# Kernel optimization log

Measured on AMD Instinct MI355X. Metric: run time of the kernel, lower is better.

Reference implementation:

```python
import jax, jax.numpy as jnp
import numpy as np

NUM_NODES = 20000
NUM_RELATIONS = 32
HIDDEN = 128
EMB = 16
NUM_EDGES = 600000


def setup_inputs() -> dict:
    key = jax.random.key(0)
    ks = jax.random.split(key, 8)
    edge_index = jax.random.randint(ks[0], (2, NUM_EDGES), 0, NUM_NODES, dtype=jnp.int64)
    edge_type = jax.random.randint(ks[1], (NUM_EDGES,), 0, NUM_RELATIONS, dtype=jnp.int64)
    node_emb = jax.random.normal(ks[2], (NUM_NODES, EMB), dtype=jnp.float32)
    W1 = jax.random.normal(ks[3], (NUM_RELATIONS, EMB, HIDDEN), dtype=jnp.float32) * (1.0 / np.sqrt(EMB))
    root1 = jax.random.normal(ks[4], (EMB, HIDDEN), dtype=jnp.float32) * (1.0 / np.sqrt(EMB))
    b1 = jnp.zeros((HIDDEN,), dtype=jnp.float32)
    W2 = jax.random.normal(ks[5], (NUM_RELATIONS, HIDDEN, HIDDEN), dtype=jnp.float32) * (1.0 / np.sqrt(HIDDEN))
    root2 = jax.random.normal(ks[6], (HIDDEN, HIDDEN), dtype=jnp.float32) * (1.0 / np.sqrt(HIDDEN))
    b2 = jnp.zeros((HIDDEN,), dtype=jnp.float32)
    return {"edge_index": edge_index, "edge_type": edge_type, "node_emb": node_emb,
            "W1": W1, "root1": root1, "b1": b1, "W2": W2, "root2": root2, "b2": b2}


def rgcn_layer(x, edge_index, edge_type, W, root, bias):
    # PyG RGCNConv: per-relation transform, per-(dst, relation) MEAN aggregation,
    # summed over relations, plus root transform and bias.
    src, dst = edge_index[0], edge_index[1]
    # mean normalization per (dst, relation) segment
    seg = dst * NUM_RELATIONS + edge_type                      # [E]
    counts = jax.ops.segment_sum(jnp.ones(seg.shape, jnp.float32), seg,
                                 num_segments=NUM_NODES * NUM_RELATIONS)
    inv = jnp.where(counts > 0, 1.0 / counts, 0.0)
    # transform every node by every relation weight: [N, R, H]
    xr = jnp.einsum('nf,rfh->nrh', x, W)
    msg = xr[src, edge_type] * inv[seg][:, None]               # [E, H]
    agg = jax.ops.segment_sum(msg, dst, num_segments=NUM_NODES)  # [N, H]
    return agg + x @ root + bias


def reference(edge_index, edge_type, node_emb, W1, root1, b1, W2, root2, b2):
    h = rgcn_layer(node_emb, edge_index, edge_type, W1, root1, b1)
    h = jax.nn.relu(h)
    h = rgcn_layer(h, edge_index, edge_type, W2, root2, b2)
    return h
```

## Files before the change

### kernel.cpp

```cpp
#include <hip/hip_runtime.h>
#include <hip/hip_bf16.h>

#define N_NODES 20000
#define N_REL 32
#define HID 128
#define EMB 16
#define N_EDGES 600000
#define NB (N_NODES * N_REL)

typedef __attribute__((ext_vector_type(8))) short  bf8v;
typedef __attribute__((ext_vector_type(8))) unsigned short us8v;
typedef __attribute__((ext_vector_type(4))) float  f4v;

__device__ __forceinline__ unsigned short f2b(float f) {
    __hip_bfloat16 h = __float2bfloat16(f);
    return __builtin_bit_cast(unsigned short, h);
}
__device__ __forceinline__ float b2f(unsigned short u) {
    unsigned int x = ((unsigned int)u) << 16;
    return __builtin_bit_cast(float, x);
}

__device__ __forceinline__ void lds_barrier() {
    asm volatile("s_waitcnt lgkmcnt(0)\n\ts_barrier" ::: "memory");
}

#define R_W2 (N_REL * HID * HID)
#define R_XB (N_NODES * EMB)
#define R_W1 (N_REL * EMB * HID)
#define R_R1 (HID * 32)
#define R_R2 (HID * HID)
#define R_HIST N_EDGES
#define PRE_TOT (R_W2 + R_XB + R_W1 + R_R1 + R_R2 + R_HIST)

__global__ __launch_bounds__(256) void pre1_k(
    const int* __restrict__ dst, const int* __restrict__ et,
    const float* __restrict__ x, const float* __restrict__ W1,
    const float* __restrict__ root1, const float* __restrict__ W2,
    const float* __restrict__ root2,
    int* __restrict__ hist,
    unsigned short* __restrict__ xb, unsigned short* __restrict__ w1t,
    unsigned short* __restrict__ r1t, unsigned short* __restrict__ w2t,
    unsigned short* __restrict__ r2t) {
    int i = blockIdx.x * 256 + threadIdx.x;
    if (i < R_W2) {
        int r = i >> 14, k = (i >> 7) & 127, n = i & 127;
        int kb = r * 4 + (k >> 5), q = (k >> 3) & 3, j = k & 7;
        int ct8 = n >> 4, m16 = n & 15;
        w2t[(size_t)kb * 4096 + ct8 * 512 + m16 * 32 + q * 8 + j] = f2b(W2[i]);
        return;
    }
    i -= R_W2;
    if (i < R_XB) { xb[i] = f2b(x[i]); return; }
    i -= R_XB;
    if (i < R_W1) {
        int rel = i >> 11, kk = (i >> 7) & 15, n = i & 127;
        int kb = rel >> 1, k = ((rel & 1) << 4) + kk;
        int q = k >> 3, j = k & 7, ct8 = n >> 4, m16 = n & 15;
        w1t[kb * 4096 + ct8 * 512 + m16 * 32 + q * 8 + j] = f2b(W1[i]);
        return;
    }
    i -= R_W1;
    if (i < R_R1) {
        int k = i >> 7, n = i & 127;
        int q = k >> 3, j = k & 7, ct8 = n >> 4, m16 = n & 15;
        r1t[ct8 * 512 + m16 * 32 + q * 8 + j] =
            (k < EMB) ? f2b(root1[k * 128 + n]) : (unsigned short)0;
        return;
    }
    i -= R_R1;
    if (i < R_R2) {
        int k = i >> 7, n = i & 127;
        int ks = k >> 5, q = (k >> 3) & 3, j = k & 7, ct8 = n >> 4, m16 = n & 15;
        r2t[(ks * 8 + ct8) * 512 + m16 * 32 + q * 8 + j] = f2b(root2[i]);
        return;
    }
    i -= R_R2;
    if (i < R_HIST) atomicAdd(&hist[dst[i] * N_REL + et[i]], 1);
}

__global__ void scan1_k(const int* __restrict__ hist, int* __restrict__ binoff,
                        int* __restrict__ cursors,
                        int* __restrict__ bsum, float* __restrict__ inv) {
    __shared__ int sh[256];
    const int t = threadIdx.x;
    const int base = blockIdx.x * 1024 + t * 4;
    int4 h4 = *(const int4*)(hist + base);
    float4 iv4;
    iv4.x = h4.x > 0 ? 1.0f / h4.x : 0.0f;
    iv4.y = h4.y > 0 ? 1.0f / h4.y : 0.0f;
    iv4.z = h4.z > 0 ? 1.0f / h4.z : 0.0f;
    iv4.w = h4.w > 0 ? 1.0f / h4.w : 0.0f;
    *(float4*)(inv + base) = iv4;
    int ts = h4.x + h4.y + h4.z + h4.w;
    sh[t] = ts;
    __syncthreads();
    for (int o = 1; o < 256; o <<= 1) {
        int v = (t >= o) ? sh[t - o] : 0;
        __syncthreads();
        sh[t] += v;
        __syncthreads();
    }
    int exc = sh[t] - ts;
    int4 b4;
    b4.x = exc;
    b4.y = exc + h4.x;
    b4.z = exc + h4.x + h4.y;
    b4.w = exc + h4.x + h4.y + h4.z;
    *(int4*)(binoff + base) = b4;
    *(int4*)(cursors + base) = b4;
    if (t == 255) bsum[blockIdx.x] = sh[255];
}

__global__ void scan2_k(const int* __restrict__ bsum, int* __restrict__ bbase,
                        int* __restrict__ binoff) {
    __shared__ int sh[1024];
    const int t = threadIdx.x;
    int v = (t < 625) ? bsum[t] : 0;
    sh[t] = v;
    __syncthreads();
    for (int o = 1; o < 1024; o <<= 1) {
        int u = (t >= o) ? sh[t - o] : 0;
        __syncthreads();
        sh[t] += u;
        __syncthreads();
    }
    if (t < 625) bbase[t] = sh[t] - v;
    if (t == 625) bbase[625] = N_EDGES;
    if (t == 626) binoff[NB] = 0;
}

__global__ void scatter_k(const int* __restrict__ src, const int* __restrict__ dst,
                          const int* __restrict__ et, int* __restrict__ cursors,
                          const int* __restrict__ bbase, int* __restrict__ ssrc) {
    int e = blockIdx.x * 256 + threadIdx.x;
    if (e < 4) ssrc[N_EDGES + e] = 0;
    if (e < N_EDGES) {
        int b = dst[e] * N_REL + et[e];
        int p = atomicAdd(&cursors[b], 1) + bbase[b >> 10];
        ssrc[p] = src[e];
    }
}

template<int ROWS, int ROWG, int NRC, int NIT, int KR, int OUT>
__global__ __launch_bounds__(256) void gemm_f(
    const int* __restrict__ binoff, const int* __restrict__ bbase,
    const float* __restrict__ inv, const int* __restrict__ ssrc,
    const unsigned short* __restrict__ G,
    const unsigned short* __restrict__ Bw,
    const unsigned short* __restrict__ Br,
    float* __restrict__ outf, unsigned short* __restrict__ fout,
    const float* __restrict__ bias) {

    constexpr int RG  = NRC * NIT;
    constexpr int KT  = (NRC * ROWG) / 32;
    constexpr int NCH = 256 / (ROWS * NRC);
    constexpr int CW  = ROWG / NCH;
    constexpr int CP8 = CW / 8;
    constexpr int LSS = NRC * ROWG + 8;
    constexpr int RT  = ROWS / 16;
    static_assert(NCH * CW == ROWG, "chunk covering must be exact");
    static_assert(CP8 * 8 == CW, "16B unit covering");
    static_assert(KT * 32 == NRC * ROWG, "K must be a multiple of 32");
    static_assert(ROWS * NRC * NCH == 256, "all threads gather");
    static_assert(RG == 32, "single group covers all relations");
    static_assert(RT * 16 == ROWS, "rows multiple of 16");

    __shared__ __align__(16) unsigned short As[2][ROWS * LSS];
    __shared__ int   smO[ROWS * (RG + 1)];
    __shared__ float smI[ROWS * RG];

    const int t = threadIdx.x;
    const int w = t >> 6, lane = t & 63;
    const int q = lane >> 4, m16 = lane & 15;
    const int d0 = blockIdx.x * ROWS;
    const int colb = w * 32;
    const int cb16 = colb >> 4;
    const int fo = m16 * 32 + q * 8;
    const int brow = t / (NRC * NCH);
    const int rsub = (t / NCH) % NRC;
    const int gcc  = t % NCH;
    const int mb  = brow * (RG + 1) + rsub;
    const int mbI = brow * RG + rsub;
    int uo[CP8];
#pragma unroll
    for (int j = 0; j < CP8; ++j) uo[j] = (gcc + j * NCH) * 8;
    const int lbase = brow * LSS + rsub * ROWG;

    for (int i = t; i < ROWS * (RG + 1); i += 256) {
        int row = i / (RG + 1), rr = i % (RG + 1);
        int bi = (d0 + row) * N_REL + rr;
        smO[i] = binoff[bi] + bbase[bi >> 10];
    }
    for (int i = t; i < ROWS * RG; i += 256) {
        int row = i / RG, rr = i % RG;
        smI[i] = inv[(d0 + row) * N_REL + rr];
    }
    lds_barrier();

    f4v acc[RT][2];
#pragma unroll
    for (int rt = 0; rt < RT; ++rt)
#pragma unroll
        for (int ct = 0; ct < 2; ++ct) acc[rt][ct] = f4v{0.f, 0.f, 0.f, 0.f};

    us8v gE[4][CP8];
#pragma unroll
    for (int e = 0; e < 4; ++e)
#pragma unroll
        for (int j = 0; j < CP8; ++j) gE[e][j] = us8v{};
    int sx[4] = {0, 0, 0, 0};

    {
        const int so = smO[mb], cnt = smO[mb + 1] - so;
        int s0 = ssrc[so], s1 = ssrc[so + 1], s2 = ssrc[so + 2], s3 = ssrc[so + 3];
        if (cnt >= 1) {
            const unsigned short* gp = G + (size_t)s0 * ROWG;
#pragma unroll
            for (int j = 0; j < CP8; ++j) gE[0][j] = *(const us8v*)(gp + uo[j]);
        }
        if (cnt >= 2) {
            const unsigned short* gp = G + (size_t)s1 * ROWG;
#pragma unroll
            for (int j = 0; j < CP8; ++j) gE[1][j] = *(const us8v*)(gp + uo[j]);
        }
        if (cnt >= 3) {
            const unsigned short* gp = G + (size_t)s2 * ROWG;
#pragma unroll
            for (int j = 0; j < CP8; ++j) gE[2][j] = *(const us8v*)(gp + uo[j]);
        }
        if (cnt >= 4) {
            const unsigned short* gp = G + (size_t)s3 * ROWG;
#pragma unroll
            for (int j = 0; j < CP8; ++j) gE[3][j] = *(const us8v*)(gp + uo[j]);
        }
        if (NIT > 1) {
            const int so1 = smO[mb + NRC];
            sx[0] = ssrc[so1]; sx[1] = ssrc[so1 + 1];
            sx[2] = ssrc[so1 + 2]; sx[3] = ssrc[so1 + 3];
        }
    }

    bf8v bfr[2][KT];
    {
#pragma unroll
        for (int ct = 0; ct < 2; ++ct) {
#pragma unroll
            for (int ks = 0; ks < KT; ++ks)
                bfr[ct][ks] = *(const bf8v*)(Bw + ((size_t)ks * 8 + cb16 + ct) * 512 + fo);
        }
    }

#pragma unroll 2
    for (int it = 0; it < NIT; ++it) {
        unsigned short* Ab = As[it & 1];
        {
            const int so = smO[mb + it * NRC], eo = smO[mb + it * NRC + 1];
            const int cnt = eo - so;
            const float m2 = cnt >= 2 ? 1.f : 0.f;
            const float m3 = cnt >= 3 ? 1.f : 0.f;
            const float m4 = cnt >= 4 ? 1.f : 0.f;
            float a[CW];
#pragma unroll
            for (int j = 0; j < CP8; ++j)
#pragma unroll
                for (int k = 0; k < 8; ++k)
                    a[j * 8 + k] = b2f(gE[0][j][k]) + m2 * b2f(gE[1][j][k])
                                 + m3 * b2f(gE[2][j][k]) + m4 * b2f(gE[3][j][k]);
            for (int p = so + 4; p < eo; ++p) {
                const unsigned short* gp = G + (size_t)ssrc[p] * ROWG;
#pragma unroll
                for (int j = 0; j < CP8; ++j) {
                    us8v g = *(const us8v*)(gp + uo[j]);
#pragma unroll
                    for (int k = 0; k < 8; ++k) a[j * 8 + k] += b2f(g[k]);
                }
            }
            const float iv = smI[mbI + it * NRC];
            unsigned short* wp = &Ab[lbase];
#pragma unroll
            for (int j = 0; j < CP8; ++j) {
                us8v sv;
#pragma unroll
                for (int k = 0; k < 8; ++k) sv[k] = f2b(a[j * 8 + k] * iv);
                *(us8v*)(wp + uo[j]) = sv;
            }

            if (it + 1 < NIT) {
                const int b1o = mb + (it + 1) * NRC;
                const int c1 = smO[b1o + 1] - smO[b1o];
                if (c1 >= 1) {
                    const unsigned short* gp = G + (size_t)sx[0] * ROWG;
#pragma unroll
                    for (int j = 0; j < CP8; ++j) gE[0][j] = *(const us8v*)(gp + uo[j]);
                }
                if (c1 >= 2) {
                    const unsigned short* gp = G + (size_t)sx[1] * ROWG;
#pragma unroll
                    for (int j = 0; j < CP8; ++j) gE[1][j] = *(const us8v*)(gp + uo[j]);
                }
                if (c1 >= 3) {
                    const unsigned short* gp = G + (size_t)sx[2] * ROWG;
#pragma unroll
                    for (int j = 0; j < CP8; ++j) gE[2][j] = *(const us8v*)(gp + uo[j]);
                }
                if (c1 >= 4) {
                    const unsigned short* gp = G + (size_t)sx[3] * ROWG;
#pragma unroll
                    for (int j = 0; j < CP8; ++j) gE[3][j] = *(const us8v*)(gp + uo[j]);
                }
                if (it + 2 < NIT) {
                    const int so2 = smO[mb + (it + 2) * NRC];
                    sx[0] = ssrc[so2]; sx[1] = ssrc[so2 + 1];
                    sx[2] = ssrc[so2 + 2]; sx[3] = ssrc[so2 + 3];
                }
            }
        }
        lds_barrier();

#pragma unroll
        for (int rt = 0; rt < RT; ++rt) {
            const unsigned short* ar = &Ab[(m16 + 16 * rt) * LSS];
#pragma unroll
            for (int ks = 0; ks < KT; ++ks) {
                bf8v af = *(const bf8v*)(ar + ks * 32 + q * 8);
                acc[rt][0] = __builtin_amdgcn_mfma_f32_16x16x32_bf16(af, bfr[0][ks], acc[rt][0], 0, 0, 0);
                acc[rt][1] = __builtin_amdgcn_mfma_f32_16x16x32_bf16(af, bfr[1][ks], acc[rt][1], 0, 0, 0);
            }
        }

        if (it + 1 < NIT) {
            const int kb0 = ((it + 1) * NRC * ROWG) >> 5;
#pragma unroll
            for (int ct = 0; ct < 2; ++ct) {
#pragma unroll
                for (int ks = 0; ks < KT; ++ks)
                    bfr[ct][ks] = *(const bf8v*)(Bw + ((size_t)(kb0 + ks) * 8 + cb16 + ct) * 512 + fo);
            }
        } else {
#pragma unroll
            for (int ct = 0; ct < 2; ++ct) {
#pragma unroll
                for (int ks = 0; ks < KR; ++ks)
                    bfr[ct][ks] = *(const bf8v*)(Br + ((size_t)ks * 8 + cb16 + ct) * 512 + fo);
            }
        }
    }

    {
#pragma unroll
        for (int rt = 0; rt < RT; ++rt) {
            const unsigned short* gr = G + (size_t)(d0 + m16 + 16 * rt) * ROWG;
#pragma unroll
            for (int ks = 0; ks < KR; ++ks) {
                bf8v af;
                if constexpr (ROWG % 32 == 0) {
                    af = *(const bf8v*)(gr + ks * 32 + q * 8);
                } else {
                    af = bf8v{0, 0, 0, 0, 0, 0, 0, 0};
                    if (ks * 32 + q * 8 + 8 <= ROWG)
                        af = *(const bf8v*)(gr + ks * 32 + q * 8);
                }
                acc[rt][0] = __builtin_amdgcn_mfma_f32_16x16x32_bf16(af, bfr[0][ks], acc[rt][0], 0, 0, 0);
                acc[rt][1] = __builtin_amdgcn_mfma_f32_16x16x32_bf16(af, bfr[1][ks], acc[rt][1], 0, 0, 0);
            }
        }
    }

    if constexpr (OUT == 1) {
#pragma unroll
        for (int ct = 0; ct < 2; ++ct) {
            const int col = colb + 16 * ct + m16;
            const float bb = bias[col];
#pragma unroll
            for (int rt = 0; rt < RT; ++rt) {
#pragma unroll
                for (int g = 0; g < 4; ++g) {
                    const int rr = 16 * rt + q * 4 + g;
                    fout[(size_t)(d0 + rr) * HID + col] =
                        f2b(fmaxf(acc[rt][ct][g] + bb, 0.0f));
                }
            }
        }
    } else {
#pragma unroll
        for (int ct = 0; ct < 2; ++ct) {
            const int col = colb + 16 * ct + m16;
            const float bb = bias[col];
#pragma unroll
            for (int rt = 0; rt < RT; ++rt) {
#pragma unroll
                for (int g = 0; g < 4; ++g) {
                    const int rr = 16 * rt + q * 4 + g;
                    outf[(size_t)(d0 + rr) * HID + col] = acc[rt][ct][g] + bb;
                }
            }
        }
    }
}

extern "C" void kernel_launch(void* const* d_in, const int* in_sizes, int n_in,
                              void* d_out, int out_size, void* d_ws, size_t ws_size,
                              hipStream_t stream) {
    const int*   ei    = (const int*)d_in[0];
    const int*   et    = (const int*)d_in[1];
    const float* x     = (const float*)d_in[2];
    const float* W1    = (const float*)d_in[3];
    const float* root1 = (const float*)d_in[4];
    const float* b1    = (const float*)d_in[5];
    const float* W2    = (const float*)d_in[6];
    const float* root2 = (const float*)d_in[7];
    const float* b2    = (const float*)d_in[8];
    float* out = (float*)d_out;

    char* ws = (char*)d_ws;
    size_t off = 0;
    auto alloc = [&](size_t bytes) { void* p = ws + off; off = (off + bytes + 63) & ~(size_t)63; return p; };
    int*   hist    = (int*)  alloc((size_t)NB * 4);
    int*   binoff  = (int*)  alloc((size_t)(NB + 1) * 4);
    int*   cursors = (int*)  alloc((size_t)NB * 4);
    float* inv     = (float*)alloc((size_t)NB * 4);
    int*   bsum    = (int*)  alloc(625 * 4);
    int*   bbase   = (int*)  alloc(626 * 4);
    int*   ssrc    = (int*)  alloc((size_t)(N_EDGES + 4) * 4);
    unsigned short* xb  = (unsigned short*)alloc((size_t)N_NODES * EMB * 2);
    unsigned short* h1b = (unsigned short*)alloc((size_t)N_NODES * HID * 2);
    unsigned short* w1t = (unsigned short*)alloc((size_t)R_W1 * 2);
    unsigned short* r1t = (unsigned short*)alloc((size_t)HID * 32 * 2);
    unsigned short* w2t = (unsigned short*)alloc((size_t)N_REL * HID * HID * 2);
    unsigned short* r2t = (unsigned short*)alloc((size_t)HID * HID * 2);

    const int* src = ei;
    const int* dst = ei + N_EDGES;

    hipMemsetAsync(hist, 0, (size_t)NB * 4, stream);
    pre1_k<<<(PRE_TOT + 255) / 256, 256, 0, stream>>>(
        dst, et, x, W1, root1, W2, root2, hist, xb, w1t, r1t, w2t, r2t);
    scan1_k<<<NB / 1024, 256, 0, stream>>>(hist, binoff, cursors, bsum, inv);
    scan2_k<<<1, 1024, 0, stream>>>(bsum, bbase, binoff);
    scatter_k<<<(N_EDGES + 255) / 256, 256, 0, stream>>>(src, dst, et, cursors, bbase, ssrc);

    gemm_f<32, 16, 8, 4, 1, 1><<<dim3(625, 1), 256, 0, stream>>>(
        binoff, bbase, inv, ssrc, xb, w1t, r1t, nullptr, h1b, b1);

    gemm_f<32, 128, 2, 16, 4, 2><<<dim3(625, 1), 256, 0, stream>>>(
        binoff, bbase, inv, ssrc, h1b, w2t, r2t, out, nullptr, b2);
}
```

Measured before the change: 262.1 us.

## Deepen gather prefetch to two stages and retune layer-2 relation chunking

The gather pipeline now keeps two register stage buffers (gA/gB) that alternate, so neighbour-row loads are issued two iterations ahead instead of one. This gives global-memory latency more time to be hidden behind the aggregation and MFMA work. Layer 2 is also relaunched with one relation per chunk and 32 iterations instead of two relations and 16 iterations, which shrinks each K-slice. The cost is roughly double the staging registers, which may lower occupancy or cause spills.

```diff
diff --git a/kernel.cpp b/kernel.cpp
--- a/kernel.cpp
+++ b/kernel.cpp
@@ -165,6 +165,7 @@
     static_assert(ROWS * NRC * NCH == 256, "all threads gather");
     static_assert(RG == 32, "single group covers all relations");
     static_assert(RT * 16 == ROWS, "rows multiple of 16");
+    static_assert(NIT % 2 == 0, "even iteration count (gA/gB alternation)");
 
     __shared__ __align__(16) unsigned short As[2][ROWS * LSS];
     __shared__ int   smO[ROWS * (RG + 1)];
@@ -204,41 +205,49 @@
 #pragma unroll
         for (int ct = 0; ct < 2; ++ct) acc[rt][ct] = f4v{0.f, 0.f, 0.f, 0.f};
 
-    us8v gE[4][CP8];
+    us8v gA[4][CP8], gB[4][CP8];
 #pragma unroll
     for (int e = 0; e < 4; ++e)
 #pragma unroll
-        for (int j = 0; j < CP8; ++j) gE[e][j] = us8v{};
+        for (int j = 0; j < CP8; ++j) { gA[e][j] = us8v{}; gB[e][j] = us8v{}; }
     int sx[4] = {0, 0, 0, 0};
+
+    auto stage4 = [&](int s0, int s1, int s2, int s3, int c,
+                      us8v (&dstE)[4][CP8]) __attribute__((always_inline)) {
+        if (c >= 1) {
+            const unsigned short* gp = G + (size_t)s0 * ROWG;
+#pragma unroll
+            for (int j = 0; j < CP8; ++j) dstE[0][j] = *(const us8v*)(gp + uo[j]);
+        }
+        if (c >= 2) {
+            const unsigned short* gp = G + (size_t)s1 * ROWG;
+#pragma unroll
+            for (int j = 0; j < CP8; ++j) dstE[1][j] = *(const us8v*)(gp + uo[j]);
+        }
+        if (c >= 3) {
+            const unsigned short* gp = G + (size_t)s2 * ROWG;
+#pragma unroll
+            for (int j = 0; j < CP8; ++j) dstE[2][j] = *(const us8v*)(gp + uo[j]);
+        }
+        if (c >= 4) {
+            const unsigned short* gp = G + (size_t)s3 * ROWG;
+#pragma unroll
+            for (int j = 0; j < CP8; ++j) dstE[3][j] = *(const us8v*)(gp + uo[j]);
+        }
+    };
 
     {
         const int so = smO[mb], cnt = smO[mb + 1] - so;
-        int s0 = ssrc[so], s1 = ssrc[so + 1], s2 = ssrc[so + 2], s3 = ssrc[so + 3];
-        if (cnt >= 1) {
-            const unsigned short* gp = G + (size_t)s0 * ROWG;
-#pragma unroll
-            for (int j = 0; j < CP8; ++j) gE[0][j] = *(const us8v*)(gp + uo[j]);
-        }
-        if (cnt >= 2) {
-            const unsigned short* gp = G + (size_t)s1 * ROWG;
-#pragma unroll
-            for (int j = 0; j < CP8; ++j) gE[1][j] = *(const us8v*)(gp + uo[j]);
-        }
-        if (cnt >= 3) {
-            const unsigned short* gp = G + (size_t)s2 * ROWG;
-#pragma unroll
-            for (int j = 0; j < CP8; ++j) gE[2][j] = *(const us8v*)(gp + uo[j]);
-        }
-        if (cnt >= 4) {
-            const unsigned short* gp = G + (size_t)s3 * ROWG;
-#pragma unroll
-            for (int j = 0; j < CP8; ++j) gE[3][j] = *(const us8v*)(gp + uo[j]);
-        }
-        if (NIT > 1) {
-            const int so1 = smO[mb + NRC];
-            sx[0] = ssrc[so1]; sx[1] = ssrc[so1 + 1];
-            sx[2] = ssrc[so1 + 2]; sx[3] = ssrc[so1 + 3];
-        }
+        stage4(ssrc[so], ssrc[so + 1], ssrc[so + 2], ssrc[so + 3], cnt, gA);
+    }
+    if (NIT > 1) {
+        const int so = smO[mb + NRC], cnt = smO[mb + NRC + 1] - so;
+        stage4(ssrc[so], ssrc[so + 1], ssrc[so + 2], ssrc[so + 3], cnt, gB);
+    }
+    if (NIT > 2) {
+        const int so = smO[mb + 2 * NRC];
+        sx[0] = ssrc[so]; sx[1] = ssrc[so + 1];
+        sx[2] = ssrc[so + 2]; sx[3] = ssrc[so + 3];
     }
 
     bf8v bfr[2][KT];
@@ -251,8 +260,7 @@
         }
     }
 
-#pragma unroll 2
-    for (int it = 0; it < NIT; ++it) {
+    auto phase = [&](int it, us8v (&cur)[4][CP8]) __attribute__((always_inline)) {
         unsigned short* Ab = As[it & 1];
         {
             const int so = smO[mb + it * NRC], eo = smO[mb + it * NRC + 1];
@@ -265,8 +273,8 @@
             for (int j = 0; j < CP8; ++j)
 #pragma unroll
                 for (int k = 0; k < 8; ++k)
-                    a[j * 8 + k] = b2f(gE[0][j][k]) + m2 * b2f(gE[1][j][k])
-                                 + m3 * b2f(gE[2][j][k]) + m4 * b2f(gE[3][j][k]);
+                    a[j * 8 + k] = b2f(cur[0][j][k]) + m2 * b2f(cur[1][j][k])
+                                 + m3 * b2f(cur[2][j][k]) + m4 * b2f(cur[3][j][k]);
             for (int p = so + 4; p < eo; ++p) {
                 const unsigned short* gp = G + (size_t)ssrc[p] * ROWG;
 #pragma unroll
@@ -286,34 +294,14 @@
                 *(us8v*)(wp + uo[j]) = sv;
             }
 
-            if (it + 1 < NIT) {
-                const int b1o = mb + (it + 1) * NRC;
-                const int c1 = smO[b1o + 1] - smO[b1o];
-                if (c1 >= 1) {
-                    const unsigned short* gp = G + (size_t)sx[0] * ROWG;
-#pragma unroll
-                    for (int j = 0; j < CP8; ++j) gE[0][j] = *(const us8v*)(gp + uo[j]);
-                }
-                if (c1 >= 2) {
-                    const unsigned short* gp = G + (size_t)sx[1] * ROWG;
-#pragma unroll
-                    for (int j = 0; j < CP8; ++j) gE[1][j] = *(const us8v*)(gp + uo[j]);
-                }
-                if (c1 >= 3) {
-                    const unsigned short* gp = G + (size_t)sx[2] * ROWG;
-#pragma unroll
-                    for (int j = 0; j < CP8; ++j) gE[2][j] = *(const us8v*)(gp + uo[j]);
-                }
-                if (c1 >= 4) {
-                    const unsigned short* gp = G + (size_t)sx[3] * ROWG;
-#pragma unroll
-                    for (int j = 0; j < CP8; ++j) gE[3][j] = *(const us8v*)(gp + uo[j]);
-                }
-                if (it + 2 < NIT) {
-                    const int so2 = smO[mb + (it + 2) * NRC];
-                    sx[0] = ssrc[so2]; sx[1] = ssrc[so2 + 1];
-                    sx[2] = ssrc[so2 + 2]; sx[3] = ssrc[so2 + 3];
-                }
+            if (it + 2 < NIT) {
+                const int b2o = mb + (it + 2) * NRC;
+                stage4(sx[0], sx[1], sx[2], sx[3], smO[b2o + 1] - smO[b2o], cur);
+            }
+            if (it + 3 < NIT) {
+                const int so3 = smO[mb + (it + 3) * NRC];
+                sx[0] = ssrc[so3]; sx[1] = ssrc[so3 + 1];
+                sx[2] = ssrc[so3 + 2]; sx[3] = ssrc[so3 + 3];
             }
         }
         lds_barrier();
@@ -345,6 +333,11 @@
                     bfr[ct][ks] = *(const bf8v*)(Br + ((size_t)ks * 8 + cb16 + ct) * 512 + fo);
             }
         }
+    };
+
+    for (int it = 0; it + 1 < NIT; it += 2) {
+        phase(it, gA);
+        phase(it + 1, gB);
     }
 
     {
@@ -443,6 +436,6 @@
     gemm_f<32, 16, 8, 4, 1, 1><<<dim3(625, 1), 256, 0, stream>>>(
         binoff, bbase, inv, ssrc, xb, w1t, r1t, nullptr, h1b, b1);
 
-    gemm_f<32, 128, 2, 16, 4, 2><<<dim3(625, 1), 256, 0, stream>>>(
+    gemm_f<32, 128, 1, 32, 4, 2><<<dim3(625, 1), 256, 0, stream>>>(
         binoff, bbase, inv, ssrc, h1b, w2t, r2t, out, nullptr, b2);
 }
```

New measurement: 256.6 us. 2.1% less time.

## Fuse preprocessing, scans and scatter into one cooperative grid-synced kernel

Applied to the files above, without the earlier changes.

Replaces the memset, conversion/histogram, two scan kernels and scatter kernel with a single cooperative kernel of 640 blocks that uses grid.sync() between phases, so four launch gaps and a memset go away. The second-level scan is now done by one 256-thread block with three elements per thread. The second GEMM template also changes its NRC/NIT split from 2x16 to 1x32. The cooperative launch needs all 640 blocks resident at once, and the grid-stride loops over a smaller grid than before may lower parallelism in the conversion phase.

```diff
diff --git a/kernel.cpp b/kernel.cpp
--- a/kernel.cpp
+++ b/kernel.cpp
@@ -1,5 +1,8 @@
 #include <hip/hip_runtime.h>
 #include <hip/hip_bf16.h>
+#include <hip/hip_cooperative_groups.h>
+
+namespace cg = cooperative_groups;
 
 #define N_NODES 20000
 #define N_REL 32
@@ -32,112 +35,124 @@
 #define R_R2 (HID * HID)
 #define R_HIST N_EDGES
 #define PRE_TOT (R_W2 + R_XB + R_W1 + R_R1 + R_R2 + R_HIST)
-
-__global__ __launch_bounds__(256) void pre1_k(
-    const int* __restrict__ dst, const int* __restrict__ et,
+#define PRE_BLOCKS 640
+
+__global__ __launch_bounds__(256) void fused_pre_k(
+    const int* __restrict__ src, const int* __restrict__ dst,
+    const int* __restrict__ et,
     const float* __restrict__ x, const float* __restrict__ W1,
     const float* __restrict__ root1, const float* __restrict__ W2,
     const float* __restrict__ root2,
-    int* __restrict__ hist,
+    int* __restrict__ hist, int* __restrict__ binoff,
+    int* __restrict__ cursors, float* __restrict__ inv,
+    int* __restrict__ bsum, int* __restrict__ bbase, int* __restrict__ ssrc,
     unsigned short* __restrict__ xb, unsigned short* __restrict__ w1t,
     unsigned short* __restrict__ r1t, unsigned short* __restrict__ w2t,
     unsigned short* __restrict__ r2t) {
-    int i = blockIdx.x * 256 + threadIdx.x;
-    if (i < R_W2) {
-        int r = i >> 14, k = (i >> 7) & 127, n = i & 127;
-        int kb = r * 4 + (k >> 5), q = (k >> 3) & 3, j = k & 7;
-        int ct8 = n >> 4, m16 = n & 15;
-        w2t[(size_t)kb * 4096 + ct8 * 512 + m16 * 32 + q * 8 + j] = f2b(W2[i]);
-        return;
-    }
-    i -= R_W2;
-    if (i < R_XB) { xb[i] = f2b(x[i]); return; }
-    i -= R_XB;
-    if (i < R_W1) {
-        int rel = i >> 11, kk = (i >> 7) & 15, n = i & 127;
-        int kb = rel >> 1, k = ((rel & 1) << 4) + kk;
-        int q = k >> 3, j = k & 7, ct8 = n >> 4, m16 = n & 15;
-        w1t[kb * 4096 + ct8 * 512 + m16 * 32 + q * 8 + j] = f2b(W1[i]);
-        return;
-    }
-    i -= R_W1;
-    if (i < R_R1) {
-        int k = i >> 7, n = i & 127;
-        int q = k >> 3, j = k & 7, ct8 = n >> 4, m16 = n & 15;
-        r1t[ct8 * 512 + m16 * 32 + q * 8 + j] =
-            (k < EMB) ? f2b(root1[k * 128 + n]) : (unsigned short)0;
-        return;
-    }
-    i -= R_R1;
-    if (i < R_R2) {
-        int k = i >> 7, n = i & 127;
-        int ks = k >> 5, q = (k >> 3) & 3, j = k & 7, ct8 = n >> 4, m16 = n & 15;
-        r2t[(ks * 8 + ct8) * 512 + m16 * 32 + q * 8 + j] = f2b(root2[i]);
-        return;
-    }
-    i -= R_R2;
-    if (i < R_HIST) atomicAdd(&hist[dst[i] * N_REL + et[i]], 1);
-}
-
-__global__ void scan1_k(const int* __restrict__ hist, int* __restrict__ binoff,
-                        int* __restrict__ cursors,
-                        int* __restrict__ bsum, float* __restrict__ inv) {
+    cg::grid_group grid = cg::this_grid();
     __shared__ int sh[256];
-    const int t = threadIdx.x;
-    const int base = blockIdx.x * 1024 + t * 4;
-    int4 h4 = *(const int4*)(hist + base);
-    float4 iv4;
-    iv4.x = h4.x > 0 ? 1.0f / h4.x : 0.0f;
-    iv4.y = h4.y > 0 ? 1.0f / h4.y : 0.0f;
-    iv4.z = h4.z > 0 ? 1.0f / h4.z : 0.0f;
-    iv4.w = h4.w > 0 ? 1.0f / h4.w : 0.0f;
-    *(float4*)(inv + base) = iv4;
-    int ts = h4.x + h4.y + h4.z + h4.w;
-    sh[t] = ts;
-    __syncthreads();
-    for (int o = 1; o < 256; o <<= 1) {
-        int v = (t >= o) ? sh[t - o] : 0;
+    const int t = threadIdx.x, b = blockIdx.x;
+    const int gtid = b * 256 + t;
+    const int GT = PRE_BLOCKS * 256;
+
+    for (int i = gtid; i < NB; i += GT) hist[i] = 0;
+    grid.sync();
+
+    for (int ii = gtid; ii < PRE_TOT; ii += GT) {
+        int i = ii;
+        if (i < R_W2) {
+            int r = i >> 14, k = (i >> 7) & 127, n = i & 127;
+            int kb = r * 4 + (k >> 5), q = (k >> 3) & 3, j = k & 7;
+            int ct8 = n >> 4, m16 = n & 15;
+            w2t[(size_t)kb * 4096 + ct8 * 512 + m16 * 32 + q * 8 + j] = f2b(W2[i]);
+            continue;
+        }
+        i -= R_W2;
+        if (i < R_XB) { xb[i] = f2b(x[i]); continue; }
+        i -= R_XB;
+        if (i < R_W1) {
+            int rel = i >> 11, kk = (i >> 7) & 15, n = i & 127;
+            int kb = rel >> 1, k = ((rel & 1) << 4) + kk;
+            int q = k >> 3, j = k & 7, ct8 = n >> 4, m16 = n & 15;
+            w1t[kb * 4096 + ct8 * 512 + m16 * 32 + q * 8 + j] = f2b(W1[i]);
+            continue;
+        }
+        i -= R_W1;
+        if (i < R_R1) {
+            int k = i >> 7, n = i & 127;
+            int q = k >> 3, j = k & 7, ct8 = n >> 4, m16 = n & 15;
+            r1t[ct8 * 512 + m16 * 32 + q * 8 + j] =
+                (k < EMB) ? f2b(root1[k * 128 + n]) : (unsigned short)0;
+            continue;
+        }
+        i -= R_R1;
+        if (i < R_R2) {
+            int k = i >> 7, n = i & 127;
+            int ks = k >> 5, q = (k >> 3) & 3, j = k & 7, ct8 = n >> 4, m16 = n & 15;
+            r2t[(ks * 8 + ct8) * 512 + m16 * 32 + q * 8 + j] = f2b(root2[i]);
+            continue;
+        }
+        i -= R_R2;
+        atomicAdd(&hist[dst[i] * N_REL + et[i]], 1);
+    }
+    grid.sync();
+
+    if (b < 625) {
+        const int base = b * 1024 + t * 4;
+        int4 h4 = *(const int4*)(hist + base);
+        float4 iv4;
+        iv4.x = h4.x > 0 ? 1.0f / h4.x : 0.0f;
+        iv4.y = h4.y > 0 ? 1.0f / h4.y : 0.0f;
+        iv4.z = h4.z > 0 ? 1.0f / h4.z : 0.0f;
+        iv4.w = h4.w > 0 ? 1.0f / h4.w : 0.0f;
+        *(float4*)(inv + base) = iv4;
+        int ts = h4.x + h4.y + h4.z + h4.w;
+        sh[t] = ts;
         __syncthreads();
-        sh[t] += v;
+        for (int o = 1; o < 256; o <<= 1) {
+            int v = (t >= o) ? sh[t - o] : 0;
+            __syncthreads();
+            sh[t] += v;
+            __syncthreads();
+        }
+        int exc = sh[t] - ts;
+        int4 b4;
+        b4.x = exc;
+        b4.y = exc + h4.x;
+        b4.z = exc + h4.x + h4.y;
+        b4.w = exc + h4.x + h4.y + h4.z;
+        *(int4*)(binoff + base) = b4;
+        *(int4*)(cursors + base) = b4;
+        if (t == 255) bsum[b] = sh[255];
+    }
+    grid.sync();
+
+    if (b == 0) {
+        const int i0 = t * 3;
+        int v0 = (i0     < 625) ? bsum[i0]     : 0;
+        int v1 = (i0 + 1 < 625) ? bsum[i0 + 1] : 0;
+        int v2 = (i0 + 2 < 625) ? bsum[i0 + 2] : 0;
+        int ps = v0 + v1 + v2;
+        sh[t] = ps;
         __syncthreads();
-    }
-    int exc = sh[t] - ts;
-    int4 b4;
-    b4.x = exc;
-    b4.y = exc + h4.x;
-    b4.z = exc + h4.x + h4.y;
-    b4.w = exc + h4.x + h4.y + h4.z;
-    *(int4*)(binoff + base) = b4;
-    *(int4*)(cursors + base) = b4;
-    if (t == 255) bsum[blockIdx.x] = sh[255];
-}
-
-__global__ void scan2_k(const int* __restrict__ bsum, int* __restrict__ bbase,
-                        int* __restrict__ binoff) {
-    __shared__ int sh[1024];
-    const int t = threadIdx.x;
-    int v = (t < 625) ? bsum[t] : 0;
-    sh[t] = v;
-    __syncthreads();
-    for (int o = 1; o < 1024; o <<= 1) {
-        int u = (t >= o) ? sh[t - o] : 0;
-        __syncthreads();
-        sh[t] += u;
-        __syncthreads();
-    }
-    if (t < 625) bbase[t] = sh[t] - v;
-    if (t == 625) bbase[625] = N_EDGES;
-    if (t == 626) binoff[NB] = 0;
-}
-
-__global__ void scatter_k(const int* __restrict__ src, const int* __restrict__ dst,
-                          const int* __restrict__ et, int* __restrict__ cursors,
-                          const int* __restrict__ bbase, int* __restrict__ ssrc) {
-    int e = blockIdx.x * 256 + threadIdx.x;
-    if (e < 4) ssrc[N_EDGES + e] = 0;
-    if (e < N_EDGES) {
-        int b = dst[e] * N_REL + et[e];
-        int p = atomicAdd(&cursors[b], 1) + bbase[b >> 10];
+        for (int o = 1; o < 256; o <<= 1) {
+            int u = (t >= o) ? sh[t - o] : 0;
+            __syncthreads();
+            sh[t] += u;
+            __syncthreads();
+        }
+        int bse = sh[t] - ps;
+        if (i0     < 625) bbase[i0]     = bse;
+        if (i0 + 1 < 625) bbase[i0 + 1] = bse + v0;
+        if (i0 + 2 < 625) bbase[i0 + 2] = bse + v0 + v1;
+        if (t == 0) { bbase[625] = N_EDGES; binoff[NB] = 0; }
+    }
+    grid.sync();
+
+    if (gtid < 4) ssrc[N_EDGES + gtid] = 0;
+    for (int e = gtid; e < N_EDGES; e += GT) {
+        int bn = dst[e] * N_REL + et[e];
+        int p = atomicAdd(&cursors[bn], 1) + bbase[bn >> 10];
         ssrc[p] = src[e];
     }
 }
@@ -433,16 +448,22 @@
     const int* src = ei;
     const int* dst = ei + N_EDGES;
 
-    hipMemsetAsync(hist, 0, (size_t)NB * 4, stream);
-    pre1_k<<<(PRE_TOT + 255) / 256, 256, 0, stream>>>(
-        dst, et, x, W1, root1, W2, root2, hist, xb, w1t, r1t, w2t, r2t);
-    scan1_k<<<NB / 1024, 256, 0, stream>>>(hist, binoff, cursors, bsum, inv);
-    scan2_k<<<1, 1024, 0, stream>>>(bsum, bbase, binoff);
-    scatter_k<<<(N_EDGES + 255) / 256, 256, 0, stream>>>(src, dst, et, cursors, bbase, ssrc);
+    {
+        void* args[] = {
+            (void*)&src, (void*)&dst, (void*)&et,
+            (void*)&x, (void*)&W1, (void*)&root1, (void*)&W2, (void*)&root2,
+            (void*)&hist, (void*)&binoff, (void*)&cursors, (void*)&inv,
+            (void*)&bsum, (void*)&bbase, (void*)&ssrc,
+            (void*)&xb, (void*)&w1t, (void*)&r1t, (void*)&w2t, (void*)&r2t
+        };
+        hipLaunchCooperativeKernel((const void*)fused_pre_k,
+                                   dim3(PRE_BLOCKS), dim3(256),
+                                   args, 0, stream);
+    }
 
     gemm_f<32, 16, 8, 4, 1, 1><<<dim3(625, 1), 256, 0, stream>>>(
         binoff, bbase, inv, ssrc, xb, w1t, r1t, nullptr, h1b, b1);
 
-    gemm_f<32, 128, 2, 16, 4, 2><<<dim3(625, 1), 256, 0, stream>>>(
+    gemm_f<32, 128, 1, 32, 4, 2><<<dim3(625, 1), 256, 0, stream>>>(
         binoff, bbase, inv, ssrc, h1b, w2t, r2t, out, nullptr, b2);
 }
```

After: 514.5 us. 96.3% more time.

## Fuse two-level scan via last-block pattern and retune layer-2 GEMM template

Applied to the files above, without the earlier changes.

Merges the second-level scan kernel into the first by having the last finishing block (detected with an atomic counter reset in the preprocessing kernel) compute the block-base prefix. This removes one kernel launch and its dependency gap. Separately, the layer-2 GEMM instantiation changes from NRC=2,NIT=16 to NRC=1,NIT=32, which alters the per-iteration K chunk and LDS staging. The GEMM body is wrapped in thin per-layer kernels. The last-block scan adds a threadfence and atomic reads.

```diff
diff --git a/kernel.cpp b/kernel.cpp
--- a/kernel.cpp
+++ b/kernel.cpp
@@ -41,8 +41,9 @@
     int* __restrict__ hist,
     unsigned short* __restrict__ xb, unsigned short* __restrict__ w1t,
     unsigned short* __restrict__ r1t, unsigned short* __restrict__ w2t,
-    unsigned short* __restrict__ r2t) {
+    unsigned short* __restrict__ r2t, int* __restrict__ done) {
     int i = blockIdx.x * 256 + threadIdx.x;
+    if (i == 0) *done = 0;
     if (i < R_W2) {
         int r = i >> 14, k = (i >> 7) & 127, n = i & 127;
         int kb = r * 4 + (k >> 5), q = (k >> 3) & 3, j = k & 7;
@@ -79,10 +80,12 @@
     if (i < R_HIST) atomicAdd(&hist[dst[i] * N_REL + et[i]], 1);
 }
 
-__global__ void scan1_k(const int* __restrict__ hist, int* __restrict__ binoff,
+__global__ void scanf_k(const int* __restrict__ hist, int* __restrict__ binoff,
                         int* __restrict__ cursors,
-                        int* __restrict__ bsum, float* __restrict__ inv) {
+                        int* __restrict__ bsum, float* __restrict__ inv,
+                        int* __restrict__ bbase, int* __restrict__ done) {
     __shared__ int sh[256];
+    __shared__ int amLast;
     const int t = threadIdx.x;
     const int base = blockIdx.x * 1024 + t * 4;
     int4 h4 = *(const int4*)(hist + base);
@@ -110,24 +113,34 @@
     *(int4*)(binoff + base) = b4;
     *(int4*)(cursors + base) = b4;
     if (t == 255) bsum[blockIdx.x] = sh[255];
-}
-
-__global__ void scan2_k(const int* __restrict__ bsum, int* __restrict__ bbase,
-                        int* __restrict__ binoff) {
-    __shared__ int sh[1024];
-    const int t = threadIdx.x;
-    int v = (t < 625) ? bsum[t] : 0;
-    sh[t] = v;
+
     __syncthreads();
-    for (int o = 1; o < 1024; o <<= 1) {
-        int u = (t >= o) ? sh[t - o] : 0;
+    if (t == 0) {
+        __threadfence();
+        amLast = (atomicAdd(done, 1) == (int)gridDim.x - 1);
+    }
+    __syncthreads();
+    if (amLast) {
+        const int i0 = t * 3;
+        int v0 = (i0     < 625) ? atomicAdd(&bsum[i0],     0) : 0;
+        int v1 = (i0 + 1 < 625) ? atomicAdd(&bsum[i0 + 1], 0) : 0;
+        int v2 = (i0 + 2 < 625) ? atomicAdd(&bsum[i0 + 2], 0) : 0;
+        int ps = v0 + v1 + v2;
         __syncthreads();
-        sh[t] += u;
+        sh[t] = ps;
         __syncthreads();
-    }
-    if (t < 625) bbase[t] = sh[t] - v;
-    if (t == 625) bbase[625] = N_EDGES;
-    if (t == 626) binoff[NB] = 0;
+        for (int o = 1; o < 256; o <<= 1) {
+            int u = (t >= o) ? sh[t - o] : 0;
+            __syncthreads();
+            sh[t] += u;
+            __syncthreads();
+        }
+        int bse = sh[t] - ps;
+        if (i0     < 625) bbase[i0]     = bse;
+        if (i0 + 1 < 625) bbase[i0 + 1] = bse + v0;
+        if (i0 + 2 < 625) bbase[i0 + 2] = bse + v0 + v1;
+        if (t == 0) { bbase[625] = N_EDGES; binoff[NB] = 0; }
+    }
 }
 
 __global__ void scatter_k(const int* __restrict__ src, const int* __restrict__ dst,
@@ -143,7 +156,7 @@
 }
 
 template<int ROWS, int ROWG, int NRC, int NIT, int KR, int OUT>
-__global__ __launch_bounds__(256) void gemm_f(
+__device__ __forceinline__ void gemm_body(
     const int* __restrict__ binoff, const int* __restrict__ bbase,
     const float* __restrict__ inv, const int* __restrict__ ssrc,
     const unsigned short* __restrict__ G,
@@ -399,6 +412,26 @@
     }
 }
 
+__global__ __launch_bounds__(256) void gemm_l1(
+    const int* __restrict__ binoff, const int* __restrict__ bbase,
+    const float* __restrict__ inv, const int* __restrict__ ssrc,
+    const unsigned short* __restrict__ G, const unsigned short* __restrict__ Bw,
+    const unsigned short* __restrict__ Br,
+    unsigned short* __restrict__ fout, const float* __restrict__ bias) {
+    gemm_body<32, 16, 8, 4, 1, 1>(binoff, bbase, inv, ssrc, G, Bw, Br,
+                                  nullptr, fout, bias);
+}
+
+__global__ __launch_bounds__(256) void gemm_l2(
+    const int* __restrict__ binoff, const int* __restrict__ bbase,
+    const float* __restrict__ inv, const int* __restrict__ ssrc,
+    const unsigned short* __restrict__ G, const unsigned short* __restrict__ Bw,
+    const unsigned short* __restrict__ Br,
+    float* __restrict__ outf, const float* __restrict__ bias) {
+    gemm_body<32, 128, 1, 32, 4, 2>(binoff, bbase, inv, ssrc, G, Bw, Br,
+                                    outf, nullptr, bias);
+}
+
 extern "C" void kernel_launch(void* const* d_in, const int* in_sizes, int n_in,
                               void* d_out, int out_size, void* d_ws, size_t ws_size,
                               hipStream_t stream) {
@@ -422,6 +455,7 @@
     float* inv     = (float*)alloc((size_t)NB * 4);
     int*   bsum    = (int*)  alloc(625 * 4);
     int*   bbase   = (int*)  alloc(626 * 4);
+    int*   done    = (int*)  alloc(64);
     int*   ssrc    = (int*)  alloc((size_t)(N_EDGES + 4) * 4);
     unsigned short* xb  = (unsigned short*)alloc((size_t)N_NODES * EMB * 2);
     unsigned short* h1b = (unsigned short*)alloc((size_t)N_NODES * HID * 2);
@@ -435,14 +469,14 @@
 
     hipMemsetAsync(hist, 0, (size_t)NB * 4, stream);
     pre1_k<<<(PRE_TOT + 255) / 256, 256, 0, stream>>>(
-        dst, et, x, W1, root1, W2, root2, hist, xb, w1t, r1t, w2t, r2t);
-    scan1_k<<<NB / 1024, 256, 0, stream>>>(hist, binoff, cursors, bsum, inv);
-    scan2_k<<<1, 1024, 0, stream>>>(bsum, bbase, binoff);
+        dst, et, x, W1, root1, W2, root2, hist, xb, w1t, r1t, w2t, r2t, done);
+    scanf_k<<<NB / 1024, 256, 0, stream>>>(hist, binoff, cursors, bsum, inv,
+                                           bbase, done);
     scatter_k<<<(N_EDGES + 255) / 256, 256, 0, stream>>>(src, dst, et, cursors, bbase, ssrc);
 
-    gemm_f<32, 16, 8, 4, 1, 1><<<dim3(625, 1), 256, 0, stream>>>(
-        binoff, bbase, inv, ssrc, xb, w1t, r1t, nullptr, h1b, b1);
-
-    gemm_f<32, 128, 2, 16, 4, 2><<<dim3(625, 1), 256, 0, stream>>>(
-        binoff, bbase, inv, ssrc, h1b, w2t, r2t, out, nullptr, b2);
-}
+    gemm_l1<<<dim3(625, 1), 256, 0, stream>>>(
+        binoff, bbase, inv, ssrc, xb, w1t, r1t, h1b, b1);
+
+    gemm_l2<<<dim3(625, 1), 256, 0, stream>>>(
+        binoff, bbase, inv, ssrc, h1b, w2t, r2t, out, b2);
+}
```

After: 247.6 us. 5.5% less time.
